# Kernel optimization log

Hardware: AMD Instinct MI355X
Metric: run time of the kernel (lower is better)

The kernel has to match this reference:

```python
import jax, jax.numpy as jnp
import numpy as np

# Architecture constants (from module defaults)
D, H, DH, P, G, DEPTH, M, NCLS = 192, 3, 64, 16, 14, 12, 128, 1000  # M = feature_map_dim // 2
EXITS = (4, 8, 12)
TEMP = 1.0 / np.sqrt(DH)  # Favor softmax_temp = 1/sqrt(d_head)
EPS_ATTN = 1e-6           # fast_transformers LinearAttention eps
LN_EPS = 1e-5


def ln(x, g, b):
    mu = x.mean(-1, keepdims=True)
    var = ((x - mu) ** 2).mean(-1, keepdims=True)
    return (x - mu) * jax.lax.rsqrt(var + LN_EPS) * g + b


def favor(x, omega):
    # FAVOR+ positive random features for the softmax kernel.
    # x: [B,L,H,DH], omega: [DH,M] -> phi: [B,L,H,2M]
    xs = x * np.float32(np.sqrt(TEMP))
    off = 0.5 * (xs * xs).sum(-1, keepdims=True)
    u = jnp.einsum('blhd,dm->blhm', xs, omega)
    phi = jnp.concatenate([jnp.exp(u - off), jnp.exp(-u - off)], axis=-1)
    return phi * np.float32(1.0 / np.sqrt(2 * M))


def forward(x, patch_w, patch_b, pe_ln_g, pe_ln_b, cls_token, pos_embed,
            Wq, bq, Wk, bk, Wv, bv, Wo, bo,
            ln1_g, ln1_b, ln2_g, ln2_b, lnb_g, lnb_b,
            W1, b1, W2, b2, omega, head_w, head_b):
    B = x.shape[0]
    # Patch embedding: Conv2d(k=16, s=16) == blocked einsum
    xp = x.reshape(B, 3, G, P, G, P)
    tok = jnp.einsum('bchpwq,dcpq->bhwd', xp, patch_w).reshape(B, G * G, D) + patch_b
    tok = ln(tok, pe_ln_g, pe_ln_b)  # PatchEmbed.norm (norm_layer=LayerNorm)
    tok = jnp.concatenate([jnp.broadcast_to(cls_token, (B, 1, D)), tok], axis=1) + pos_embed
    xc = tok  # [B, 197, D]
    outs = []
    for i in range(DEPTH):
        # --- linear (FAVOR) attention ---
        q = (xc @ Wq[i].T + bq[i]).reshape(B, -1, H, DH)
        k = (xc @ Wk[i].T + bk[i]).reshape(B, -1, H, DH)
        v = (xc @ Wv[i].T + bv[i]).reshape(B, -1, H, DH)
        Qp = favor(q, omega[i])
        Kp = favor(k, omega[i])
        KV = jnp.einsum('bshm,bshd->bhmd', Kp, v)
        Z = 1.0 / (jnp.einsum('blhm,bhm->blh', Qp, Kp.sum(axis=1)) + EPS_ATTN)
        attn = jnp.einsum('blhm,bhmd,blh->blhd', Qp, KV, Z).reshape(B, -1, D)
        # fast_transformers TransformerEncoderLayer (post-norm style)
        xc = xc + attn @ Wo[i].T + bo[i]
        y = xc = ln(xc, ln1_g[i], ln1_b[i])
        y = jax.nn.relu(y @ W1[i].T + b1[i]) @ W2[i].T + b2[i]
        xc = ln(xc + y, ln2_g[i], ln2_b[i])
        # per-block TransformerEncoder final norm (builder final_normalization)
        xc = ln(xc, lnb_g[i], lnb_b[i])
        if (i + 1) in EXITS:
            j = EXITS.index(i + 1)
            z = xc.mean(axis=1)  # AdaptiveAvgPool1d(1) over sequence
            outs.append(z @ head_w[j].T + head_b[j])
    return tuple(outs)


def setup_inputs() -> dict:
    key = jax.random.key(0)
    ks = iter(jax.random.split(key, 32))
    n = lambda shape, s=0.02: jax.random.normal(next(ks), shape, jnp.float32) * s
    return dict(
        x=jax.random.normal(next(ks), (64, 3, 224, 224), jnp.float32),
        patch_w=n((D, 3, P, P)), patch_b=jnp.zeros((D,), jnp.float32),
        pe_ln_g=jnp.ones((D,), jnp.float32), pe_ln_b=jnp.zeros((D,), jnp.float32),
        cls_token=n((1, 1, D)), pos_embed=n((1, G * G + 1, D)),
        Wq=n((DEPTH, D, D)), bq=jnp.zeros((DEPTH, D), jnp.float32),
        Wk=n((DEPTH, D, D)), bk=jnp.zeros((DEPTH, D), jnp.float32),
        Wv=n((DEPTH, D, D)), bv=jnp.zeros((DEPTH, D), jnp.float32),
        Wo=n((DEPTH, D, D)), bo=jnp.zeros((DEPTH, D), jnp.float32),
        ln1_g=jnp.ones((DEPTH, D), jnp.float32), ln1_b=jnp.zeros((DEPTH, D), jnp.float32),
        ln2_g=jnp.ones((DEPTH, D), jnp.float32), ln2_b=jnp.zeros((DEPTH, D), jnp.float32),
        lnb_g=jnp.ones((DEPTH, D), jnp.float32), lnb_b=jnp.zeros((DEPTH, D), jnp.float32),
        W1=n((DEPTH, 4 * D, D)), b1=jnp.zeros((DEPTH, 4 * D), jnp.float32),
        W2=n((DEPTH, D, 4 * D)), b2=jnp.zeros((DEPTH, D), jnp.float32),
        omega=jax.random.normal(next(ks), (DEPTH, DH, M), jnp.float32),
        head_w=n((len(EXITS), NCLS, D)), head_b=jnp.zeros((len(EXITS), NCLS), jnp.float32),
    )


def reference(x, patch_w, patch_b, pe_ln_g, pe_ln_b, cls_token, pos_embed,
              Wq, bq, Wk, bk, Wv, bv, Wo, bo,
              ln1_g, ln1_b, ln2_g, ln2_b, lnb_g, lnb_b,
              W1, b1, W2, b2, omega, head_w, head_b):
    return forward(x, patch_w, patch_b, pe_ln_g, pe_ln_b, cls_token, pos_embed,
                   Wq, bq, Wk, bk, Wv, bv, Wo, bo,
                   ln1_g, ln1_b, ln2_g, ln2_b, lnb_g, lnb_b,
                   W1, b1, W2, b2, omega, head_w, head_b)
```

## Files before the change

### kernel.cpp

```cpp
#include <hip/hip_runtime.h>
#include <math.h>

#define BB     64
#define LLEN   197
#define BLROWS 12608
#define MPAD   12672
#define DMODEL 192
#define NHEAD  3
#define DHEAD  64
#define M2FEAT 256
#define FFDIM  768
#define NDEPTH 12
#define NCLS   1000
#define NPATCH 196
#define BPROWS 12544
#define KPATCH 768
#define PHIRS  264

#define MODE_PLAIN 0
#define MODE_RELU  1
#define MODE_PART  3

typedef unsigned short ushort;
typedef __attribute__((ext_vector_type(8))) short bf16x8;
typedef __attribute__((ext_vector_type(4))) float floatx4;
typedef __attribute__((ext_vector_type(4))) short short4v;

__device__ __forceinline__ float wave_reduce_sum(float v) {
#pragma unroll
  for (int s = 32; s > 0; s >>= 1) v += __shfl_xor(v, s, 64);
  return v;
}
__device__ __forceinline__ ushort f2bf(float f) {
  unsigned u = __float_as_uint(f);
  return (ushort)((u + 0x7fffu + ((u >> 16) & 1u)) >> 16);
}
__device__ __forceinline__ float bf2f(ushort u) {
  return __uint_as_float(((unsigned)u) << 16);
}
__device__ __forceinline__ void gll16(const ushort* g, ushort* l) {
  __builtin_amdgcn_global_load_lds(
      (const __attribute__((address_space(1))) void*)g,
      (__attribute__((address_space(3))) void*)l, 16, 0, 0);
}

__global__ __launch_bounds__(256) void gemm_128(
    const ushort* __restrict__ A, int lda,
    const ushort* __restrict__ W, int ldw,
    const float* __restrict__ bias,
    ushort* __restrict__ C, int ldc, int Ndim, int Kdim, int mode)
{
  __shared__ __align__(16) ushort As[2][128 * 32];
  __shared__ __align__(16) ushort Ws[2][128 * 32];
  const int tid = threadIdx.x;
  const int bm = blockIdx.x, bn = blockIdx.y;
  const int wave = tid >> 6, lane = tid & 63;
  const int wm = (wave >> 1) * 64, wn = (wave & 1) * 64;
  const int quad = lane >> 4, l16 = lane & 15;
  const int lrow = lane >> 2, lk = (lane & 3) * 8;
  const ushort* Ap = A + (size_t)(bm * 128) * lda;
  const ushort* Wp = W + (size_t)(bn * 128) * ldw;
  floatx4 acc[4][4] = {};
  const int nT = Kdim >> 5;
#pragma unroll
  for (int t = 0; t < 2; ++t) {
    const int rb = (t * 4 + wave) * 16;
    gll16(Ap + (size_t)(rb + lrow) * lda + lk, &As[0][rb * 32]);
    gll16(Wp + (size_t)(rb + lrow) * ldw + lk, &Ws[0][rb * 32]);
  }
  for (int kt = 0; kt < nT; ++kt) {
    const int cur = kt & 1;
    __syncthreads();
    if (kt + 1 < nT) {
      const int kk = (kt + 1) * 32, nxt = cur ^ 1;
#pragma unroll
      for (int t = 0; t < 2; ++t) {
        const int rb = (t * 4 + wave) * 16;
        gll16(Ap + (size_t)(rb + lrow) * lda + kk + lk, &As[nxt][rb * 32]);
        gll16(Wp + (size_t)(rb + lrow) * ldw + kk + lk, &Ws[nxt][rb * 32]);
      }
    }
    bf16x8 af[4], bf[4];
#pragma unroll
    for (int i = 0; i < 4; ++i) {
      af[i] = *(const bf16x8*)&As[cur][(wm + i * 16 + l16) * 32 + quad * 8];
      bf[i] = *(const bf16x8*)&Ws[cur][(wn + i * 16 + l16) * 32 + quad * 8];
    }
#pragma unroll
    for (int i = 0; i < 4; ++i)
#pragma unroll
      for (int j = 0; j < 4; ++j)
        acc[i][j] = __builtin_amdgcn_mfma_f32_16x16x32_bf16(af[i], bf[j], acc[i][j], 0, 0, 0);
  }
#pragma unroll
  for (int j = 0; j < 4; ++j) {
    const int col = bn * 128 + wn + j * 16 + l16;
    if (col >= Ndim) continue;
    const float bv = bias[col];
#pragma unroll
    for (int i = 0; i < 4; ++i)
#pragma unroll
      for (int r = 0; r < 4; ++r) {
        const int grow = bm * 128 + wm + i * 16 + quad * 4 + r;
        float o = acc[i][j][r] + bv;
        if (mode == MODE_RELU) o = fmaxf(o, 0.f);
        C[(size_t)grow * ldc + col] = f2bf(o);
      }
  }
}

__global__ __launch_bounds__(256) void gemm_bf2(
    const ushort* __restrict__ A, int lda,
    const ushort* __restrict__ W, int ldw,
    const float* __restrict__ bias,
    ushort* __restrict__ C, float* __restrict__ P, int ldc,
    int Kchunk, int mode)
{
  __shared__ __align__(16) ushort As[2][128 * 32];
  __shared__ __align__(16) ushort Ws[2][64 * 32];
  const int tid = threadIdx.x;
  const int bm = blockIdx.x, bn = blockIdx.y, bz = blockIdx.z;
  const int wave = tid >> 6, lane = tid & 63;
  const int wm = (wave >> 1) * 64, wn = (wave & 1) * 32;
  const int quad = lane >> 4, l16 = lane & 15;
  const int lrow = lane >> 2, lk = (lane & 3) * 8;
  const ushort* Ap = A + (size_t)(bm * 128) * lda + bz * Kchunk;
  const ushort* Wp = W + (size_t)(bn * 64) * ldw + bz * Kchunk;
  floatx4 acc[4][2] = {};
  const int nT = Kchunk >> 5;
#pragma unroll
  for (int t = 0; t < 2; ++t) {
    const int rb = (t * 4 + wave) * 16;
    gll16(Ap + (size_t)(rb + lrow) * lda + lk, &As[0][rb * 32]);
  }
  gll16(Wp + (size_t)(wave * 16 + lrow) * ldw + lk, &Ws[0][wave * 16 * 32]);
  for (int kt = 0; kt < nT; ++kt) {
    const int cur = kt & 1;
    __syncthreads();
    if (kt + 1 < nT) {
      const int kk = (kt + 1) * 32, nxt = cur ^ 1;
#pragma unroll
      for (int t = 0; t < 2; ++t) {
        const int rb = (t * 4 + wave) * 16;
        gll16(Ap + (size_t)(rb + lrow) * lda + kk + lk, &As[nxt][rb * 32]);
      }
      gll16(Wp + (size_t)(wave * 16 + lrow) * ldw + kk + lk, &Ws[nxt][wave * 16 * 32]);
    }
    bf16x8 af[4], bf[2];
#pragma unroll
    for (int i = 0; i < 4; ++i)
      af[i] = *(const bf16x8*)&As[cur][(wm + i * 16 + l16) * 32 + quad * 8];
#pragma unroll
    for (int j = 0; j < 2; ++j)
      bf[j] = *(const bf16x8*)&Ws[cur][(wn + j * 16 + l16) * 32 + quad * 8];
#pragma unroll
    for (int i = 0; i < 4; ++i)
#pragma unroll
      for (int j = 0; j < 2; ++j)
        acc[i][j] = __builtin_amdgcn_mfma_f32_16x16x32_bf16(af[i], bf[j], acc[i][j], 0, 0, 0);
  }
  if (mode == MODE_PART) {
#pragma unroll
    for (int j = 0; j < 2; ++j) {
      const int col = bn * 64 + wn + j * 16 + l16;
#pragma unroll
      for (int i = 0; i < 4; ++i)
#pragma unroll
        for (int r = 0; r < 4; ++r) {
          const int grow = bm * 128 + wm + i * 16 + quad * 4 + r;
          P[((size_t)bz * MPAD + grow) * ldc + col] = acc[i][j][r];
        }
    }
  } else {
#pragma unroll
    for (int j = 0; j < 2; ++j) {
      const int col = bn * 64 + wn + j * 16 + l16;
      const float bv = bias[col];
#pragma unroll
      for (int i = 0; i < 4; ++i)
#pragma unroll
        for (int r = 0; r < 4; ++r) {
          const int grow = bm * 128 + wm + i * 16 + quad * 4 + r;
          float o = acc[i][j][r] + bv;
          if (mode == MODE_RELU) o = fmaxf(o, 0.f);
          C[(size_t)grow * ldc + col] = f2bf(o);
        }
    }
  }
}

__global__ __launch_bounds__(256) void kv_fused(
    const ushort* __restrict__ qkv, const ushort* __restrict__ OmT,
    ushort* __restrict__ KVt)
{
  __shared__ __align__(16) ushort Ks[32 * 64];
  __shared__ __align__(16) ushort Vs[32 * 64];
  __shared__ __align__(16) ushort Om[64 * 64];
  __shared__ __align__(16) ushort PhT[128 * 32];
  __shared__ __align__(16) ushort Vts[80 * 32];
  __shared__ float offs[32];
  const int tid = threadIdx.x;
  const int bh = blockIdx.x, mh = blockIdx.y;
  const int b = bh / 3, h = bh - b * 3;
  const int wave = tid >> 6, lane = tid & 63;
  const int quad = lane >> 4, l16 = lane & 15;
  const int lr8 = lane >> 3, lk8 = (lane & 7) * 8;
#pragma unroll
  for (int t = 0; t < 2; ++t) {
    const int rb = (t * 4 + wave) * 8;
    gll16(OmT + (size_t)(mh * 64 + rb + lr8) * 64 + lk8, &Om[rb * 64]);
  }
  {
    const int rb = wave * 8;
    const int l = rb + lr8;
    gll16(qkv + (size_t)(b * 197 + l) * 576 + 192 + h * 64 + lk8, &Ks[rb * 64]);
    gll16(qkv + (size_t)(b * 197 + l) * 576 + 384 + h * 64 + lk8, &Vs[rb * 64]);
  }
  floatx4 acc[2][5] = {};
  for (int c = 0; c < 7; ++c) {
    const int l0 = c * 32;
    __syncthreads();
    if (tid < 64) {
      const int row = tid >> 1, half = tid & 1;
      float s = 0.f;
#pragma unroll
      for (int t = 0; t < 4; ++t) {
        bf16x8 v8 = *(const bf16x8*)&Ks[row * 64 + half * 32 + t * 8];
#pragma unroll
        for (int q = 0; q < 8; ++q) { float xv = bf2f((ushort)v8[q]); s += xv * xv; }
      }
      s += __shfl_xor(s, 1, 64);
      if (half == 0) offs[row] = 0.0625f * s;
    }
    for (int e = tid; e < 80 * 32; e += 256) {
      const int d = e >> 5, ll = e & 31;
      ushort v = 0;
      if (l0 + ll < 197) {
        if (d < 64) v = Vs[ll * 64 + d];
        else if (d == 64) v = 0x3F80;
      }
      Vts[d * 32 + ll] = v;
    }
    floatx4 ui[2] = {};
#pragma unroll
    for (int ks = 0; ks < 64; ks += 32) {
      bf16x8 af[2], bfm;
#pragma unroll
      for (int i = 0; i < 2; ++i)
        af[i] = *(const bf16x8*)&Ks[(i * 16 + l16) * 64 + ks + quad * 8];
      bfm = *(const bf16x8*)&Om[(wave * 16 + l16) * 64 + ks + quad * 8];
#pragma unroll
      for (int i = 0; i < 2; ++i)
        ui[i] = __builtin_amdgcn_mfma_f32_16x16x32_bf16(af[i], bfm, ui[i], 0, 0, 0);
    }
    __syncthreads();
    {
      const int mloc = wave * 16 + l16;
#pragma unroll
      for (int i = 0; i < 2; ++i) {
#pragma unroll
        for (int r = 0; r < 4; ++r) {
          const int ll = i * 16 + quad * 4 + r;
          float ep = 0.f, em = 0.f;
          if (l0 + ll < 197) {
            const float off = offs[ll];
            const float u = ui[i][r];
            ep = __expf(u - off) * 0.0625f;
            em = __expf(-u - off) * 0.0625f;
          }
          PhT[mloc * 32 + ll] = f2bf(ep);
          PhT[(64 + mloc) * 32 + ll] = f2bf(em);
        }
      }
    }
    if (c + 1 < 7) {
      const int rb = wave * 8;
      const int l = (c + 1) * 32 + rb + lr8;
      gll16(qkv + (size_t)(b * 197 + l) * 576 + 192 + h * 64 + lk8, &Ks[rb * 64]);
      gll16(qkv + (size_t)(b * 197 + l) * 576 + 384 + h * 64 + lk8, &Vs[rb * 64]);
    }
    __syncthreads();
    bf16x8 af[2], bf[5];
#pragma unroll
    for (int i = 0; i < 2; ++i)
      af[i] = *(const bf16x8*)&PhT[(wave * 32 + i * 16 + l16) * 32 + quad * 8];
#pragma unroll
    for (int j = 0; j < 5; ++j)
      bf[j] = *(const bf16x8*)&Vts[(j * 16 + l16) * 32 + quad * 8];
#pragma unroll
    for (int i = 0; i < 2; ++i)
#pragma unroll
      for (int j = 0; j < 5; ++j)
        acc[i][j] = __builtin_amdgcn_mfma_f32_16x16x32_bf16(af[i], bf[j], acc[i][j], 0, 0, 0);
  }
#pragma unroll
  for (int i = 0; i < 2; ++i) {
    const int prow0 = wave * 32 + i * 16 + quad * 4;
    const int f0 = (prow0 < 64) ? (mh * 64 + prow0) : (128 + mh * 64 + prow0 - 64);
#pragma unroll
    for (int j = 0; j < 5; ++j) {
      const int d = j * 16 + l16;
      short4v pk;
#pragma unroll
      for (int r = 0; r < 4; ++r) pk[r] = (short)f2bf(acc[i][j][r]);
      *(short4v*)(KVt + ((size_t)bh * 80 + d) * 256 + f0) = pk;
    }
  }
}

__global__ __launch_bounds__(256) void attn_fused(
    const ushort* __restrict__ qkv, const ushort* __restrict__ OmT,
    const ushort* __restrict__ KVt, ushort* __restrict__ OUT)
{
  __shared__ __align__(16) ushort Phi[128 * PHIRS];
  __shared__ __align__(16) ushort Bs[2][80 * 32];
  __shared__ float offs[128];
  __shared__ float zs[128];
  ushort* Qs = Phi;
  ushort* Om = Phi + 128 * 64;
  const int tid = threadIdx.x;
  const int bx = blockIdx.x, bh = blockIdx.y;
  const int b = bh / 3, h = bh - b * 3;
  const int wave = tid >> 6, lane = tid & 63;
  const int wm = (wave >> 1) * 64, wn = (wave & 1) * 64;
  const int quad = lane >> 4, l16 = lane & 15;
  const int lr8 = lane >> 3, lk8 = (lane & 7) * 8;
  const int lrow = lane >> 2, lk = (lane & 3) * 8;
#pragma unroll
  for (int t = 0; t < 4; ++t) {
    const int rb = (t * 4 + wave) * 8;
    const int l = bx * 128 + rb + lr8;
    gll16(qkv + (size_t)(b * 197 + l) * 576 + h * 64 + lk8, &Qs[rb * 64]);
    gll16(OmT + (size_t)(rb + lr8) * 64 + lk8, &Om[rb * 64]);
  }
  __syncthreads();
  {
    const int row = tid >> 1, half = tid & 1;
    float s = 0.f;
#pragma unroll
    for (int t = 0; t < 4; ++t) {
      bf16x8 v8 = *(const bf16x8*)&Qs[row * 64 + half * 32 + t * 8];
#pragma unroll
      for (int q = 0; q < 8; ++q) { float xv = bf2f((ushort)v8[q]); s += xv * xv; }
    }
    s += __shfl_xor(s, 1, 64);
    if (half == 0) offs[row] = 0.0625f * s;
  }
  floatx4 uacc[4][4] = {};
#pragma unroll
  for (int ks = 0; ks < 64; ks += 32) {
    bf16x8 af[4], bf[4];
#pragma unroll
    for (int i = 0; i < 4; ++i) {
      af[i] = *(const bf16x8*)&Qs[(wm + i * 16 + l16) * 64 + ks + quad * 8];
      bf[i] = *(const bf16x8*)&Om[(wn + i * 16 + l16) * 64 + ks + quad * 8];
    }
#pragma unroll
    for (int i = 0; i < 4; ++i)
#pragma unroll
      for (int j = 0; j < 4; ++j)
        uacc[i][j] = __builtin_amdgcn_mfma_f32_16x16x32_bf16(af[i], bf[j], uacc[i][j], 0, 0, 0);
  }
  __syncthreads();
#pragma unroll
  for (int i = 0; i < 4; ++i) {
#pragma unroll
    for (int r = 0; r < 4; ++r) {
      const int l = wm + i * 16 + quad * 4 + r;
      const float off = offs[l];
#pragma unroll
      for (int j = 0; j < 4; ++j) {
        const int m = wn + j * 16 + l16;
        const float u = uacc[i][j][r];
        Phi[l * PHIRS + m]       = f2bf(__expf(u - off)  * 0.0625f);
        Phi[l * PHIRS + m + 128] = f2bf(__expf(-u - off) * 0.0625f);
      }
    }
  }
  const ushort* Bp = KVt + (size_t)bh * 80 * 256;
  gll16(Bp + (size_t)(wave * 16 + lrow) * 256 + lk, &Bs[0][wave * 16 * 32]);
  if (wave == 0) gll16(Bp + (size_t)(64 + lrow) * 256 + lk, &Bs[0][64 * 32]);
  floatx4 acc[2][5] = {};
  for (int c = 0; c < 8; ++c) {
    const int cur = c & 1;
    __syncthreads();
    if (c + 1 < 8) {
      const int m0 = (c + 1) * 32, nxt = cur ^ 1;
      gll16(Bp + (size_t)(wave * 16 + lrow) * 256 + m0 + lk, &Bs[nxt][wave * 16 * 32]);
      if (wave == 0) gll16(Bp + (size_t)(64 + lrow) * 256 + m0 + lk, &Bs[nxt][64 * 32]);
    }
    const int m0 = c * 32;
    bf16x8 af[2], bf[5];
#pragma unroll
    for (int i = 0; i < 2; ++i)
      af[i] = *(const bf16x8*)&Phi[(wave * 32 + i * 16 + l16) * PHIRS + m0 + quad * 8];
#pragma unroll
    for (int j = 0; j < 5; ++j)
      bf[j] = *(const bf16x8*)&Bs[cur][(j * 16 + l16) * 32 + quad * 8];
#pragma unroll
    for (int i = 0; i < 2; ++i)
#pragma unroll
      for (int j = 0; j < 5; ++j)
        acc[i][j] = __builtin_amdgcn_mfma_f32_16x16x32_bf16(af[i], bf[j], acc[i][j], 0, 0, 0);
  }
  if (l16 == 0) {
#pragma unroll
    for (int i = 0; i < 2; ++i)
#pragma unroll
      for (int r = 0; r < 4; ++r)
        zs[wave * 32 + i * 16 + quad * 4 + r] = acc[i][4][r];
  }
  __syncthreads();
#pragma unroll
  for (int i = 0; i < 2; ++i) {
#pragma unroll
    for (int r = 0; r < 4; ++r) {
      const int ll = wave * 32 + i * 16 + quad * 4 + r;
      const int l = bx * 128 + ll;
      if (l >= 197) continue;
      const float z = 1.f / (zs[ll] + 1e-6f);
#pragma unroll
      for (int j = 0; j < 4; ++j)
        OUT[(size_t)(b * 197 + l) * 192 + h * 64 + j * 16 + l16] =
            f2bf(acc[i][j][r] * z);
    }
  }
}

__global__ void conv_qkv(const float* __restrict__ Wq, const float* __restrict__ Wk,
                         const float* __restrict__ Wv, const float* __restrict__ bq,
                         const float* __restrict__ bk, const float* __restrict__ bv,
                         ushort* __restrict__ dst, float* __restrict__ bdst) {
  const int l = blockIdx.y;
  const int e = blockIdx.x * 256 + threadIdx.x;
  const int n = e / 192, k = e - n * 192;
  const float* src;
  if (n < 192)      src = Wq + (size_t)l * 36864 + n * 192;
  else if (n < 384) src = Wk + (size_t)l * 36864 + (n - 192) * 192;
  else              src = Wv + (size_t)l * 36864 + (n - 384) * 192;
  dst[(size_t)l * 640 * 192 + e] = f2bf(src[k]);
  if (e < 576) {
    float bvv;
    if (e < 192)      bvv = bq[l * 192 + e];
    else if (e < 384) bvv = bk[l * 192 + e - 192];
    else              bvv = bv[l * 192 + e - 384];
    bdst[l * 576 + e] = bvv;
  }
}

__global__ void conv_pad(const float* __restrict__ src, ushort* __restrict__ dst,
                         int NK, int padNK) {
  const int l = blockIdx.y;
  const int e = blockIdx.x * 256 + threadIdx.x;
  if (e < NK) dst[(size_t)l * padNK + e] = f2bf(src[(size_t)l * NK + e]);
}

__global__ void conv_omt(const float* __restrict__ om, ushort* __restrict__ dst) {
  const int l = blockIdx.y;
  const int e = blockIdx.x * 256 + threadIdx.x;
  const int m = e >> 6, d = e & 63;
  dst[(size_t)l * 8192 + e] = f2bf(0.35355339059327379f * om[(size_t)l * 8192 + d * 128 + m]);
}

__global__ __launch_bounds__(256) void im2col_kernel(
    const float* __restrict__ X, ushort* __restrict__ Apd)
{
  const int bp = blockIdx.x;
  const int b = bp / NPATCH, p = bp - b * NPATCH;
  const int gh = p / 14, gw = p - gh * 14;
  for (int e = threadIdx.x; e < KPATCH; e += 256) {
    const int c = e >> 8, rem = e & 255, ph = rem >> 4, pw = rem & 15;
    Apd[(size_t)bp * KPATCH + e] =
        f2bf(X[((size_t)(b * 3 + c) * 224 + gh * 16 + ph) * 224 + gw * 16 + pw]);
  }
}

__global__ __launch_bounds__(256) void assemble_kernel(
    const ushort* __restrict__ TK, const float* __restrict__ g,
    const float* __restrict__ bt, const float* __restrict__ cls,
    const float* __restrict__ pos, ushort* __restrict__ XC)
{
  const int w = threadIdx.x >> 6, lane = threadIdx.x & 63;
  const int row = blockIdx.x * 4 + w;
  const int b = row / LLEN, l = row - b * LLEN;
  float o0, o1, o2;
  if (l == 0) {
    o0 = cls[lane]; o1 = cls[lane + 64]; o2 = cls[lane + 128];
  } else {
    const ushort* tp = TK + (size_t)(b * NPATCH + l - 1) * DMODEL;
    const float x0 = bf2f(tp[lane]), x1 = bf2f(tp[lane + 64]), x2 = bf2f(tp[lane + 128]);
    const float s  = wave_reduce_sum(x0 + x1 + x2);
    const float sq = wave_reduce_sum(x0 * x0 + x1 * x1 + x2 * x2);
    const float mu = s * (1.f / 192.f);
    const float var = sq * (1.f / 192.f) - mu * mu;
    const float rs = rsqrtf(var + 1e-5f);
    o0 = (x0 - mu) * rs * g[lane]       + bt[lane];
    o1 = (x1 - mu) * rs * g[lane + 64]  + bt[lane + 64];
    o2 = (x2 - mu) * rs * g[lane + 128] + bt[lane + 128];
  }
  o0 += pos[l * DMODEL + lane];
  o1 += pos[l * DMODEL + lane + 64];
  o2 += pos[l * DMODEL + lane + 128];
  ushort* xp = XC + (size_t)row * DMODEL;
  xp[lane] = f2bf(o0); xp[lane + 64] = f2bf(o1); xp[lane + 128] = f2bf(o2);
}

__global__ __launch_bounds__(256) void ln1_fused(
    ushort* __restrict__ XC, const float* __restrict__ P,
    const float* __restrict__ bias,
    const float* __restrict__ g, const float* __restrict__ bt)
{
  const int w = threadIdx.x >> 6, lane = threadIdx.x & 63;
  const int row = blockIdx.x * 4 + w;
  ushort* xp = XC + (size_t)row * DMODEL;
  const float* p0 = P + (size_t)row * DMODEL;
  const float* p1 = P + ((size_t)MPAD + row) * DMODEL;
  const float x0 = bf2f(xp[lane])       + p0[lane]       + p1[lane]       + bias[lane];
  const float x1 = bf2f(xp[lane + 64])  + p0[lane + 64]  + p1[lane + 64]  + bias[lane + 64];
  const float x2 = bf2f(xp[lane + 128]) + p0[lane + 128] + p1[lane + 128] + bias[lane + 128];
  const float s  = wave_reduce_sum(x0 + x1 + x2);
  const float sq = wave_reduce_sum(x0 * x0 + x1 * x1 + x2 * x2);
  const float mu = s * (1.f / 192.f);
  const float var = sq * (1.f / 192.f) - mu * mu;
  const float rs = rsqrtf(var + 1e-5f);
  xp[lane]       = f2bf((x0 - mu) * rs * g[lane]       + bt[lane]);
  xp[lane + 64]  = f2bf((x1 - mu) * rs * g[lane + 64]  + bt[lane + 64]);
  xp[lane + 128] = f2bf((x2 - mu) * rs * g[lane + 128] + bt[lane + 128]);
}

__global__ __launch_bounds__(256) void ln2_fused(
    ushort* __restrict__ XC, const float* __restrict__ P,
    const float* __restrict__ bias,
    const float* __restrict__ ga, const float* __restrict__ ba,
    const float* __restrict__ gb, const float* __restrict__ bb)
{
  const int w = threadIdx.x >> 6, lane = threadIdx.x & 63;
  const int row = blockIdx.x * 4 + w;
  ushort* xp = XC + (size_t)row * DMODEL;
  const float* p0 = P + (size_t)row * DMODEL;
  const float* p1 = P + ((size_t)MPAD + row) * DMODEL;
  float x0 = bf2f(xp[lane])       + p0[lane]       + p1[lane]       + bias[lane];
  float x1 = bf2f(xp[lane + 64])  + p0[lane + 64]  + p1[lane + 64]  + bias[lane + 64];
  float x2 = bf2f(xp[lane + 128]) + p0[lane + 128] + p1[lane + 128] + bias[lane + 128];
  {
    const float s  = wave_reduce_sum(x0 + x1 + x2);
    const float sq = wave_reduce_sum(x0 * x0 + x1 * x1 + x2 * x2);
    const float mu = s * (1.f / 192.f);
    const float var = sq * (1.f / 192.f) - mu * mu;
    const float rs = rsqrtf(var + 1e-5f);
    x0 = (x0 - mu) * rs * ga[lane]       + ba[lane];
    x1 = (x1 - mu) * rs * ga[lane + 64]  + ba[lane + 64];
    x2 = (x2 - mu) * rs * ga[lane + 128] + ba[lane + 128];
  }
  const float s  = wave_reduce_sum(x0 + x1 + x2);
  const float sq = wave_reduce_sum(x0 * x0 + x1 * x1 + x2 * x2);
  const float mu = s * (1.f / 192.f);
  const float var = sq * (1.f / 192.f) - mu * mu;
  const float rs = rsqrtf(var + 1e-5f);
  xp[lane]       = f2bf((x0 - mu) * rs * gb[lane]       + bb[lane]);
  xp[lane + 64]  = f2bf((x1 - mu) * rs * gb[lane + 64]  + bb[lane + 64]);
  xp[lane + 128] = f2bf((x2 - mu) * rs * gb[lane + 128] + bb[lane + 128]);
}

__global__ __launch_bounds__(192) void pool_kernel(
    const ushort* __restrict__ XC, float* __restrict__ Zp)
{
  const int b = blockIdx.x, d = threadIdx.x;
  float s = 0.f;
#pragma unroll 4
  for (int l = 0; l < LLEN; ++l) s += bf2f(XC[(size_t)(b * LLEN + l) * DMODEL + d]);
  Zp[b * DMODEL + d] = s * (1.f / 197.f);
}

__global__ __launch_bounds__(256) void head_kernel(
    const float* __restrict__ Zp, const float* __restrict__ HW,
    const float* __restrict__ HB, float* __restrict__ OUTp)
{
  const int n = blockIdx.x * 256 + threadIdx.x;
  const int b = blockIdx.y;
  if (n < NCLS) {
    const float* z = Zp + b * DMODEL;
    const float* w = HW + (size_t)n * DMODEL;
    float s = HB[n];
#pragma unroll 4
    for (int d = 0; d < DMODEL; ++d) s = fmaf(z[d], w[d], s);
    OUTp[(size_t)b * NCLS + n] = s;
  }
}

extern "C" void kernel_launch(void* const* d_in, const int* in_sizes, int n_in,
                              void* d_out, int out_size, void* d_ws, size_t ws_size,
                              hipStream_t stream) {
  const float* x        = (const float*)d_in[0];
  const float* patch_w  = (const float*)d_in[1];
  const float* patch_b  = (const float*)d_in[2];
  const float* pe_ln_g  = (const float*)d_in[3];
  const float* pe_ln_b  = (const float*)d_in[4];
  const float* cls_tok  = (const float*)d_in[5];
  const float* pos_emb  = (const float*)d_in[6];
  const float* Wq = (const float*)d_in[7];
  const float* bq = (const float*)d_in[8];
  const float* Wk = (const float*)d_in[9];
  const float* bk = (const float*)d_in[10];
  const float* Wv = (const float*)d_in[11];
  const float* bv = (const float*)d_in[12];
  const float* Wo = (const float*)d_in[13];
  const float* bo = (const float*)d_in[14];
  const float* ln1_g = (const float*)d_in[15];
  const float* ln1_b = (const float*)d_in[16];
  const float* ln2_g = (const float*)d_in[17];
  const float* ln2_b = (const float*)d_in[18];
  const float* lnb_g = (const float*)d_in[19];
  const float* lnb_b = (const float*)d_in[20];
  const float* W1 = (const float*)d_in[21];
  const float* b1 = (const float*)d_in[22];
  const float* W2 = (const float*)d_in[23];
  const float* b2 = (const float*)d_in[24];
  const float* omega  = (const float*)d_in[25];
  const float* head_w = (const float*)d_in[26];
  const float* head_b = (const float*)d_in[27];
  float* out = (float*)d_out;
  char* wsb = (char*)d_ws;

  size_t off = 0;
  auto carve = [&](size_t bytes) { size_t o = off; off += (bytes + 255) & ~(size_t)255; return o; };
  ushort* xc     = (ushort*)(wsb + carve((size_t)MPAD * 192 * 2));
  ushort* qkv    = (ushort*)(wsb + carve((size_t)MPAD * 576 * 2));
  ushort* ab     = (ushort*)(wsb + carve((size_t)MPAD * 192 * 2));
  ushort* hidden = (ushort*)(wsb + carve((size_t)MPAD * 768 * 2));
  ushort* KVt    = (ushort*)(wsb + carve((size_t)192 * 80 * 256 * 2));
  float*  Pbuf   = (float*)(wsb + carve((size_t)2 * MPAD * 192 * 4));
  float*  ZPb    = (float*)(wsb + carve((size_t)64 * 192 * 4));
  float*  bqkv   = (float*)(wsb + carve((size_t)12 * 576 * 4));
  ushort* Wqkv_bf = (ushort*)(wsb + carve((size_t)12 * 640 * 192 * 2));
  ushort* Wo_bf   = (ushort*)(wsb + carve((size_t)12 * 256 * 192 * 2));
  ushort* W1_bf   = (ushort*)(wsb + carve((size_t)12 * 768 * 192 * 2));
  ushort* W2_bf   = (ushort*)(wsb + carve((size_t)12 * 256 * 768 * 2));
  ushort* Wp_bf   = (ushort*)(wsb + carve((size_t)256 * 768 * 2));
  ushort* Om_bf   = (ushort*)(wsb + carve((size_t)12 * 128 * 64 * 2));
  ushort* i2c     = hidden;

  conv_qkv<<<dim3(432, 12), 256, 0, stream>>>(Wq, Wk, Wv, bq, bk, bv, Wqkv_bf, bqkv);
  conv_pad<<<dim3(144, 12), 256, 0, stream>>>(Wo, Wo_bf, 36864, 256 * 192);
  conv_pad<<<dim3(576, 12), 256, 0, stream>>>(W1, W1_bf, 147456, 768 * 192);
  conv_pad<<<dim3(576, 12), 256, 0, stream>>>(W2, W2_bf, 147456, 256 * 768);
  conv_pad<<<dim3(576, 1), 256, 0, stream>>>(patch_w, Wp_bf, 147456, 256 * 768);
  conv_omt<<<dim3(32, 12), 256, 0, stream>>>(omega, Om_bf);

  im2col_kernel<<<BPROWS, 256, 0, stream>>>(x, i2c);
  gemm_bf2<<<dim3(98, 3, 1), 256, 0, stream>>>(i2c, KPATCH, Wp_bf, KPATCH,
      patch_b, ab, nullptr, DMODEL, KPATCH, MODE_PLAIN);
  assemble_kernel<<<BLROWS / 4, 256, 0, stream>>>(ab, pe_ln_g, pe_ln_b,
                                                  cls_tok, pos_emb, xc);

  const int exits[3] = {3, 7, 11};
  for (int i = 0; i < NDEPTH; ++i) {
    gemm_128<<<dim3(99, 5), 256, 0, stream>>>(xc, DMODEL,
        Wqkv_bf + (size_t)i * 640 * 192, DMODEL, bqkv + i * 576,
        qkv, 576, 576, DMODEL, MODE_PLAIN);
    kv_fused<<<dim3(192, 2), 256, 0, stream>>>(qkv,
        Om_bf + (size_t)i * 8192, KVt);
    attn_fused<<<dim3(2, 192), 256, 0, stream>>>(qkv,
        Om_bf + (size_t)i * 8192, KVt, ab);
    gemm_bf2<<<dim3(99, 3, 2), 256, 0, stream>>>(ab, DMODEL,
        Wo_bf + (size_t)i * 256 * 192, DMODEL, nullptr,
        nullptr, Pbuf, DMODEL, 96, MODE_PART);
    ln1_fused<<<BLROWS / 4, 256, 0, stream>>>(xc, Pbuf, bo + i * DMODEL,
        ln1_g + i * DMODEL, ln1_b + i * DMODEL);
    gemm_128<<<dim3(99, 6), 256, 0, stream>>>(xc, DMODEL,
        W1_bf + (size_t)i * 768 * 192, DMODEL, b1 + i * FFDIM,
        hidden, FFDIM, FFDIM, DMODEL, MODE_RELU);
    gemm_bf2<<<dim3(99, 3, 2), 256, 0, stream>>>(hidden, FFDIM,
        W2_bf + (size_t)i * 256 * 768, FFDIM, nullptr,
        nullptr, Pbuf, DMODEL, 384, MODE_PART);
    ln2_fused<<<BLROWS / 4, 256, 0, stream>>>(xc, Pbuf, b2 + i * DMODEL,
        ln2_g + i * DMODEL, ln2_b + i * DMODEL,
        lnb_g + i * DMODEL, lnb_b + i * DMODEL);

    for (int j = 0; j < 3; ++j) {
      if (i == exits[j]) {
        pool_kernel<<<BB, 192, 0, stream>>>(xc, ZPb);
        head_kernel<<<dim3(4, BB), 256, 0, stream>>>(
            ZPb, head_w + (size_t)j * NCLS * DMODEL, head_b + (size_t)j * NCLS,
            out + (size_t)j * BB * NCLS);
      }
    }
  }
}
```

Before: 1.622 ms.

## Fuse Wo and W2 GEMMs with residual add and LayerNorm epilogue

Replaces the split-K Wo and W2 GEMMs, which wrote fp32 partials, and the separate ln1/ln2 kernels with one gemm_ln kernel. Each block computes 64 full rows of 192 columns, then adds bias and the residual and applies one or two LayerNorms in registers before writing bf16 back to xc. This removes the fp32 partial buffer traffic and two launches per layer. In exchange the grid shrinks to 198 blocks with no split-K, so fewer CUs are busy during the long-K W2 GEMM.

```diff
diff --git a/kernel.cpp b/kernel.cpp
--- a/kernel.cpp
+++ b/kernel.cpp
@@ -19,7 +19,6 @@
 
 #define MODE_PLAIN 0
 #define MODE_RELU  1
-#define MODE_PART  3
 
 typedef unsigned short ushort;
 typedef __attribute__((ext_vector_type(8))) short bf16x8;
@@ -113,21 +112,20 @@
     const ushort* __restrict__ A, int lda,
     const ushort* __restrict__ W, int ldw,
     const float* __restrict__ bias,
-    ushort* __restrict__ C, float* __restrict__ P, int ldc,
-    int Kchunk, int mode)
+    ushort* __restrict__ C, int ldc, int Kdim, int mode)
 {
   __shared__ __align__(16) ushort As[2][128 * 32];
   __shared__ __align__(16) ushort Ws[2][64 * 32];
   const int tid = threadIdx.x;
-  const int bm = blockIdx.x, bn = blockIdx.y, bz = blockIdx.z;
+  const int bm = blockIdx.x, bn = blockIdx.y;
   const int wave = tid >> 6, lane = tid & 63;
   const int wm = (wave >> 1) * 64, wn = (wave & 1) * 32;
   const int quad = lane >> 4, l16 = lane & 15;
   const int lrow = lane >> 2, lk = (lane & 3) * 8;
-  const ushort* Ap = A + (size_t)(bm * 128) * lda + bz * Kchunk;
-  const ushort* Wp = W + (size_t)(bn * 64) * ldw + bz * Kchunk;
+  const ushort* Ap = A + (size_t)(bm * 128) * lda;
+  const ushort* Wp = W + (size_t)(bn * 64) * ldw;
   floatx4 acc[4][2] = {};
-  const int nT = Kchunk >> 5;
+  const int nT = Kdim >> 5;
 #pragma unroll
   for (int t = 0; t < 2; ++t) {
     const int rb = (t * 4 + wave) * 16;
@@ -159,33 +157,109 @@
       for (int j = 0; j < 2; ++j)
         acc[i][j] = __builtin_amdgcn_mfma_f32_16x16x32_bf16(af[i], bf[j], acc[i][j], 0, 0, 0);
   }
-  if (mode == MODE_PART) {
-#pragma unroll
-    for (int j = 0; j < 2; ++j) {
-      const int col = bn * 64 + wn + j * 16 + l16;
-#pragma unroll
-      for (int i = 0; i < 4; ++i)
-#pragma unroll
-        for (int r = 0; r < 4; ++r) {
-          const int grow = bm * 128 + wm + i * 16 + quad * 4 + r;
-          P[((size_t)bz * MPAD + grow) * ldc + col] = acc[i][j][r];
-        }
-    }
-  } else {
-#pragma unroll
-    for (int j = 0; j < 2; ++j) {
-      const int col = bn * 64 + wn + j * 16 + l16;
-      const float bv = bias[col];
-#pragma unroll
-      for (int i = 0; i < 4; ++i)
-#pragma unroll
-        for (int r = 0; r < 4; ++r) {
-          const int grow = bm * 128 + wm + i * 16 + quad * 4 + r;
-          float o = acc[i][j][r] + bv;
-          if (mode == MODE_RELU) o = fmaxf(o, 0.f);
-          C[(size_t)grow * ldc + col] = f2bf(o);
-        }
-    }
+#pragma unroll
+  for (int j = 0; j < 2; ++j) {
+    const int col = bn * 64 + wn + j * 16 + l16;
+    const float bv = bias[col];
+#pragma unroll
+    for (int i = 0; i < 4; ++i)
+#pragma unroll
+      for (int r = 0; r < 4; ++r) {
+        const int grow = bm * 128 + wm + i * 16 + quad * 4 + r;
+        float o = acc[i][j][r] + bv;
+        if (mode == MODE_RELU) o = fmaxf(o, 0.f);
+        C[(size_t)grow * ldc + col] = f2bf(o);
+      }
+  }
+}
+
+__global__ __launch_bounds__(256) void gemm_ln(
+    const ushort* __restrict__ A, int lda,
+    const ushort* __restrict__ W, int ldw,
+    const float* __restrict__ bias,
+    ushort* __restrict__ XC,
+    const float* __restrict__ ga, const float* __restrict__ ba,
+    const float* __restrict__ gb, const float* __restrict__ bb,
+    int Kdim, int dln)
+{
+  __shared__ __align__(16) ushort As[2][64 * 32];
+  __shared__ __align__(16) ushort Ws[2][192 * 32];
+  const int tid = threadIdx.x;
+  const int bm = blockIdx.x;
+  const int wave = tid >> 6, lane = tid & 63;
+  const int quad = lane >> 4, l16 = lane & 15;
+  const int lrow = lane >> 2, lk = (lane & 3) * 8;
+  const ushort* Ap = A + (size_t)(bm * 64) * lda;
+  floatx4 acc[12] = {};
+  const int nT = Kdim >> 5;
+  gll16(Ap + (size_t)(wave * 16 + lrow) * lda + lk, &As[0][wave * 16 * 32]);
+#pragma unroll
+  for (int t = 0; t < 3; ++t) {
+    const int rb = wave * 48 + t * 16;
+    gll16(W + (size_t)(rb + lrow) * ldw + lk, &Ws[0][rb * 32]);
+  }
+  for (int kt = 0; kt < nT; ++kt) {
+    const int cur = kt & 1;
+    __syncthreads();
+    if (kt + 1 < nT) {
+      const int kk = (kt + 1) * 32, nxt = cur ^ 1;
+      gll16(Ap + (size_t)(wave * 16 + lrow) * lda + kk + lk, &As[nxt][wave * 16 * 32]);
+#pragma unroll
+      for (int t = 0; t < 3; ++t) {
+        const int rb = wave * 48 + t * 16;
+        gll16(W + (size_t)(rb + lrow) * ldw + kk + lk, &Ws[nxt][rb * 32]);
+      }
+    }
+    const bf16x8 af = *(const bf16x8*)&As[cur][(wave * 16 + l16) * 32 + quad * 8];
+#pragma unroll
+    for (int j = 0; j < 12; ++j) {
+      const bf16x8 bf = *(const bf16x8*)&Ws[cur][(j * 16 + l16) * 32 + quad * 8];
+      acc[j] = __builtin_amdgcn_mfma_f32_16x16x32_bf16(af, bf, acc[j], 0, 0, 0);
+    }
+  }
+#pragma unroll
+  for (int r = 0; r < 4; ++r) {
+    const int row = bm * 64 + wave * 16 + quad * 4 + r;
+    ushort* xp = XC + (size_t)row * DMODEL;
+    float xr[12];
+    float s = 0.f, sq = 0.f;
+#pragma unroll
+    for (int j = 0; j < 12; ++j) {
+      const int col = j * 16 + l16;
+      const float o = acc[j][r] + bias[col] + bf2f(xp[col]);
+      xr[j] = o; s += o; sq += o * o;
+    }
+#pragma unroll
+    for (int m = 1; m < 16; m <<= 1) {
+      s += __shfl_xor(s, m, 64); sq += __shfl_xor(sq, m, 64);
+    }
+    float mu = s * (1.f / 192.f);
+    float var = sq * (1.f / 192.f) - mu * mu;
+    float rs = rsqrtf(var + 1e-5f);
+#pragma unroll
+    for (int j = 0; j < 12; ++j) {
+      const int col = j * 16 + l16;
+      xr[j] = (xr[j] - mu) * rs * ga[col] + ba[col];
+    }
+    if (dln) {
+      float s2 = 0.f, sq2 = 0.f;
+#pragma unroll
+      for (int j = 0; j < 12; ++j) { s2 += xr[j]; sq2 += xr[j] * xr[j]; }
+#pragma unroll
+      for (int m = 1; m < 16; m <<= 1) {
+        s2 += __shfl_xor(s2, m, 64); sq2 += __shfl_xor(sq2, m, 64);
+      }
+      mu = s2 * (1.f / 192.f);
+      var = sq2 * (1.f / 192.f) - mu * mu;
+      rs = rsqrtf(var + 1e-5f);
+#pragma unroll
+      for (int j = 0; j < 12; ++j) {
+        const int col = j * 16 + l16;
+        xr[j] = (xr[j] - mu) * rs * gb[col] + bb[col];
+      }
+    }
+#pragma unroll
+    for (int j = 0; j < 12; ++j) xp[j * 16 + l16] = f2bf(xr[j]);
   }
 }
 
@@ -503,63 +577,6 @@
   o2 += pos[l * DMODEL + lane + 128];
   ushort* xp = XC + (size_t)row * DMODEL;
   xp[lane] = f2bf(o0); xp[lane + 64] = f2bf(o1); xp[lane + 128] = f2bf(o2);
-}
-
-__global__ __launch_bounds__(256) void ln1_fused(
-    ushort* __restrict__ XC, const float* __restrict__ P,
-    const float* __restrict__ bias,
-    const float* __restrict__ g, const float* __restrict__ bt)
-{
-  const int w = threadIdx.x >> 6, lane = threadIdx.x & 63;
-  const int row = blockIdx.x * 4 + w;
-  ushort* xp = XC + (size_t)row * DMODEL;
-  const float* p0 = P + (size_t)row * DMODEL;
-  const float* p1 = P + ((size_t)MPAD + row) * DMODEL;
-  const float x0 = bf2f(xp[lane])       + p0[lane]       + p1[lane]       + bias[lane];
-  const float x1 = bf2f(xp[lane + 64])  + p0[lane + 64]  + p1[lane + 64]  + bias[lane + 64];
-  const float x2 = bf2f(xp[lane + 128]) + p0[lane + 128] + p1[lane + 128] + bias[lane + 128];
-  const float s  = wave_reduce_sum(x0 + x1 + x2);
-  const float sq = wave_reduce_sum(x0 * x0 + x1 * x1 + x2 * x2);
-  const float mu = s * (1.f / 192.f);
-  const float var = sq * (1.f / 192.f) - mu * mu;
-  const float rs = rsqrtf(var + 1e-5f);
-  xp[lane]       = f2bf((x0 - mu) * rs * g[lane]       + bt[lane]);
-  xp[lane + 64]  = f2bf((x1 - mu) * rs * g[lane + 64]  + bt[lane + 64]);
-  xp[lane + 128] = f2bf((x2 - mu) * rs * g[lane + 128] + bt[lane + 128]);
-}
-
-__global__ __launch_bounds__(256) void ln2_fused(
-    ushort* __restrict__ XC, const float* __restrict__ P,
-    const float* __restrict__ bias,
-    const float* __restrict__ ga, const float* __restrict__ ba,
-    const float* __restrict__ gb, const float* __restrict__ bb)
-{
-  const int w = threadIdx.x >> 6, lane = threadIdx.x & 63;
-  const int row = blockIdx.x * 4 + w;
-  ushort* xp = XC + (size_t)row * DMODEL;
-  const float* p0 = P + (size_t)row * DMODEL;
-  const float* p1 = P + ((size_t)MPAD + row) * DMODEL;
-  float x0 = bf2f(xp[lane])       + p0[lane]       + p1[lane]       + bias[lane];
-  float x1 = bf2f(xp[lane + 64])  + p0[lane + 64]  + p1[lane + 64]  + bias[lane + 64];
-  float x2 = bf2f(xp[lane + 128]) + p0[lane + 128] + p1[lane + 128] + bias[lane + 128];
-  {
-    const float s  = wave_reduce_sum(x0 + x1 + x2);
-    const float sq = wave_reduce_sum(x0 * x0 + x1 * x1 + x2 * x2);
-    const float mu = s * (1.f / 192.f);
-    const float var = sq * (1.f / 192.f) - mu * mu;
-    const float rs = rsqrtf(var + 1e-5f);
-    x0 = (x0 - mu) * rs * ga[lane]       + ba[lane];
-    x1 = (x1 - mu) * rs * ga[lane + 64]  + ba[lane + 64];
-    x2 = (x2 - mu) * rs * ga[lane + 128] + ba[lane + 128];
-  }
-  const float s  = wave_reduce_sum(x0 + x1 + x2);
-  const float sq = wave_reduce_sum(x0 * x0 + x1 * x1 + x2 * x2);
-  const float mu = s * (1.f / 192.f);
-  const float var = sq * (1.f / 192.f) - mu * mu;
-  const float rs = rsqrtf(var + 1e-5f);
-  xp[lane]       = f2bf((x0 - mu) * rs * gb[lane]       + bb[lane]);
-  xp[lane + 64]  = f2bf((x1 - mu) * rs * gb[lane + 64]  + bb[lane + 64]);
-  xp[lane + 128] = f2bf((x2 - mu) * rs * gb[lane + 128] + bb[lane + 128]);
 }
 
 __global__ __launch_bounds__(192) void pool_kernel(
@@ -629,7 +646,6 @@
   ushort* ab     = (ushort*)(wsb + carve((size_t)MPAD * 192 * 2));
   ushort* hidden = (ushort*)(wsb + carve((size_t)MPAD * 768 * 2));
   ushort* KVt    = (ushort*)(wsb + carve((size_t)192 * 80 * 256 * 2));
-  float*  Pbuf   = (float*)(wsb + carve((size_t)2 * MPAD * 192 * 4));
   float*  ZPb    = (float*)(wsb + carve((size_t)64 * 192 * 4));
   float*  bqkv   = (float*)(wsb + carve((size_t)12 * 576 * 4));
   ushort* Wqkv_bf = (ushort*)(wsb + carve((size_t)12 * 640 * 192 * 2));
@@ -648,8 +664,8 @@
   conv_omt<<<dim3(32, 12), 256, 0, stream>>>(omega, Om_bf);
 
   im2col_kernel<<<BPROWS, 256, 0, stream>>>(x, i2c);
-  gemm_bf2<<<dim3(98, 3, 1), 256, 0, stream>>>(i2c, KPATCH, Wp_bf, KPATCH,
-      patch_b, ab, nullptr, DMODEL, KPATCH, MODE_PLAIN);
+  gemm_bf2<<<dim3(98, 3), 256, 0, stream>>>(i2c, KPATCH, Wp_bf, KPATCH,
+      patch_b, ab, DMODEL, KPATCH, MODE_PLAIN);
   assemble_kernel<<<BLROWS / 4, 256, 0, stream>>>(ab, pe_ln_g, pe_ln_b,
                                                   cls_tok, pos_emb, xc);
 
@@ -662,20 +678,19 @@
         Om_bf + (size_t)i * 8192, KVt);
     attn_fused<<<dim3(2, 192), 256, 0, stream>>>(qkv,
         Om_bf + (size_t)i * 8192, KVt, ab);
-    gemm_bf2<<<dim3(99, 3, 2), 256, 0, stream>>>(ab, DMODEL,
-        Wo_bf + (size_t)i * 256 * 192, DMODEL, nullptr,
-        nullptr, Pbuf, DMODEL, 96, MODE_PART);
-    ln1_fused<<<BLROWS / 4, 256, 0, stream>>>(xc, Pbuf, bo + i * DMODEL,
-        ln1_g + i * DMODEL, ln1_b + i * DMODEL);
+    gemm_ln<<<MPAD / 64, 256, 0, stream>>>(ab, DMODEL,
+        Wo_bf + (size_t)i * 256 * 192, DMODEL, bo + i * DMODEL, xc,
+        ln1_g + i * DMODEL, ln1_b + i * DMODEL, nullptr, nullptr,
+        DMODEL, 0);
     gemm_128<<<dim3(99, 6), 256, 0, stream>>>(xc, DMODEL,
         W1_bf + (size_t)i * 768 * 192, DMODEL, b1 + i * FFDIM,
         hidden, FFDIM, FFDIM, DMODEL, MODE_RELU);
-    gemm_bf2<<<dim3(99, 3, 2), 256, 0, stream>>>(hidden, FFDIM,
-        W2_bf + (size_t)i * 256 * 768, FFDIM, nullptr,
-        nullptr, Pbuf, DMODEL, 384, MODE_PART);
-    ln2_fused<<<BLROWS / 4, 256, 0, stream>>>(xc, Pbuf, b2 + i * DMODEL,
+    gemm_ln<<<MPAD / 64, 256, 0, stream>>>(hidden, FFDIM,
+        W2_bf + (size_t)i * 256 * 768, FFDIM, b2 + i * DMODEL, xc,
         ln2_g + i * DMODEL, ln2_b + i * DMODEL,
-        lnb_g + i * DMODEL, lnb_b + i * DMODEL);
+        lnb_g + i * DMODEL, lnb_b + i * DMODEL,
+        FFDIM, 1);
+    ln2_fusedless:;
 
     for (int j = 0; j < 3; ++j) {
       if (i == exits[j]) {
```

New measurement: 1.614 ms. About the same (-0.5%).
